# Kernel tuning notes

Hardware: AMD Instinct MI355X
Metric: run time of the kernel (lower is better)

## Reference

```python
import jax, jax.numpy as jnp
import numpy as np

BS, N_LINKS, MAX_LEN = 8192, 512, 32
D_LINK, D_PATH, D_READ, N_OUT = 32, 128, 256, 3
BN_EPS = 1e-5


def setup_inputs() -> dict:
    key = jax.random.key(0)
    ks = jax.random.split(key, 16)
    capa = jax.random.uniform(ks[0], (BS, N_LINKS), jnp.float32, 0.5, 1.0) * 100.0
    avail = jax.random.uniform(ks[1], (BS, N_LINKS), jnp.float32) * capa
    loss = jax.random.uniform(ks[2], (BS, N_LINKS), jnp.float32) * 0.05
    demand = jax.random.uniform(ks[3], (BS,), jnp.float32) * 10.0
    path = jax.random.randint(ks[4], (BS, MAX_LEN), 0, N_LINKS)
    hop_num = jax.random.randint(ks[5], (BS,), 1, MAX_LEN + 1)
    s = 0.1
    inp = {
        "demand": demand,
        "link_avail_capacity": avail,
        "link_capacity": capa,
        "link_loss": loss,
        "path": path,
        "hop_num": hop_num,
        # GRU params (PyTorch layout: [3H, D] gates ordered r,z,n)
        "gru_w_ih": jax.random.normal(ks[6], (3 * D_PATH, D_LINK), jnp.float32) * s,
        "gru_w_hh": jax.random.normal(ks[7], (3 * D_PATH, D_PATH), jnp.float32) * s,
        "gru_b_ih": jax.random.normal(ks[8], (3 * D_PATH,), jnp.float32) * s,
        "gru_b_hh": jax.random.normal(ks[9], (3 * D_PATH,), jnp.float32) * s,
        "bn_gamma": jnp.ones((D_PATH,), jnp.float32),
        "bn_beta": jnp.zeros((D_PATH,), jnp.float32),
        # stacked readout heads [N_OUT, ...]
        "rW1": jax.random.normal(ks[10], (N_OUT, D_PATH, D_READ), jnp.float32) * s,
        "rb1": jnp.zeros((N_OUT, D_READ), jnp.float32),
        "rW2": jax.random.normal(ks[11], (N_OUT, D_READ, D_READ), jnp.float32) * s,
        "rb2": jnp.zeros((N_OUT, D_READ), jnp.float32),
        "rW3": jax.random.normal(ks[12], (N_OUT, D_READ, 1), jnp.float32) * s,
        "rb3": jnp.zeros((N_OUT, 1), jnp.float32),
    }
    return inp


def _gru_scan(x_bt, h0, w_ih, w_hh, b_ih, b_hh):
    # x_bt: [B, T, D]; h0: [B, H] -> outputs [B, T, H]
    H = h0.shape[-1]
    def step(h, x_t):
        gi = x_t @ w_ih.T + b_ih          # [B, 3H]
        gh = h @ w_hh.T + b_hh            # [B, 3H]
        i_r, i_z, i_n = gi[:, :H], gi[:, H:2*H], gi[:, 2*H:]
        h_r, h_z, h_n = gh[:, :H], gh[:, H:2*H], gh[:, 2*H:]
        r = jax.nn.sigmoid(i_r + h_r)
        z = jax.nn.sigmoid(i_z + h_z)
        n = jnp.tanh(i_n + r * h_n)
        h_new = (1.0 - z) * n + z * h
        return h_new, h_new
    _, outs = jax.lax.scan(step, h0, jnp.swapaxes(x_bt, 0, 1))
    return jnp.swapaxes(outs, 0, 1)


def reference(demand, link_avail_capacity, link_capacity, link_loss, path, hop_num,
              gru_w_ih, gru_w_hh, gru_b_ih, gru_b_hh, bn_gamma, bn_beta,
              rW1, rb1, rW2, rb2, rW3, rb3):
    bs, n_links = link_capacity.shape
    max_len = path.shape[1]
    max_capa = jax.lax.stop_gradient(jnp.max(link_capacity))
    # link_state: [B, n_links, D_LINK]; first D_LINK-4 channels are zeros
    feats = jnp.stack([
        link_avail_capacity / max_capa,
        link_capacity / max_capa,
        link_avail_capacity / link_capacity,
        link_loss,
    ], axis=-1)
    link_state = jnp.concatenate(
        [jnp.zeros((bs, n_links, D_LINK - 4), feats.dtype), feats], axis=-1)
    link_state = jax.lax.stop_gradient(link_state)  # original detaches
    # initial hidden: zeros except last channel = demand/max_capa
    h0 = jnp.concatenate(
        [jnp.zeros((bs, D_PATH - 1), feats.dtype), (demand / max_capa)[:, None]], axis=-1)
    # fused gather of link states along each path, masked past hop_num
    gathered = jnp.take_along_axis(link_state, path[:, :, None], axis=1)  # [B, T, D]
    mask = (jnp.arange(max_len)[None, :] < hop_num[:, None])[:, :, None]
    link_inputs = gathered * mask.astype(gathered.dtype)
    outputs = _gru_scan(link_inputs, h0, gru_w_ih, gru_w_hh, gru_b_ih, gru_b_hh)
    # extract hidden state at last hop of each path
    idx = (hop_num - 1)[:, None, None]
    flow = jnp.take_along_axis(outputs, idx, axis=1)[:, 0, :]  # [B, H]
    # BatchNorm1d (training mode: batch statistics, biased variance)
    mean = jnp.mean(flow, axis=0)
    var = jnp.mean((flow - mean) ** 2, axis=0)
    flow = (flow - mean) * jax.lax.rsqrt(var + BN_EPS) * bn_gamma + bn_beta
    # readout heads: Linear -> SELU -> Linear -> SELU -> Linear
    h1 = jax.nn.selu(jnp.einsum('bh,uhr->ubr', flow, rW1) + rb1[:, None, :])
    h2 = jax.nn.selu(jnp.einsum('ubr,urs->ubs', h1, rW2) + rb2[:, None, :])
    y = jnp.einsum('ubs,uso->ubo', h2, rW3) + rb3[:, None, :]  # [U, B, 1]
    return jnp.transpose(y[:, :, 0], (1, 0))  # [B, U]
```

## Files before the change

### kernel.cpp

```cpp
#include <hip/hip_runtime.h>


#define BS 8192
#define NL 512
#define ML 32
#define DP 128
#define DR 256
#define NJOB 512
#define ST 172

#define OFF_SUM    64
#define OFF_SSQ    192
#define OFF_CUR    576
#define OFF_PERM   640
#define OFF_WHH16  (OFF_PERM + BS)
#define OFF_W1     (OFF_WHH16 + 24576)
#define OFF_W2     (OFF_W1 + 49152)
#define OFF_FEATS  (OFF_W2 + 98304)
#define OFF_FLOW   (OFF_FEATS + BS*ML*4)

#define FEATS_BLOCKS 1024
#define MAX_BLOCKS   256
#define WPREP_BLOCKS 336
#define SORT_BID     (FEATS_BLOCKS + MAX_BLOCKS + WPREP_BLOCKS)
#define PREP_GRID    (SORT_BID + 1)

#define KS (-1.44269504088896340736f)
#define KT ( 2.88539008177792681472f)

typedef _Float16 f16x8 __attribute__((ext_vector_type(8)));
typedef _Float16 f16x4 __attribute__((ext_vector_type(4)));
typedef float    f32x4 __attribute__((ext_vector_type(4)));

__device__ __forceinline__ float exp2_raw_(float x){
#if __has_builtin(__builtin_amdgcn_exp2f)
  return __builtin_amdgcn_exp2f(x);
#else
  return exp2f(x);
#endif
}

__device__ __forceinline__ float sig2_(float x){
  return __builtin_amdgcn_rcpf(1.0f + exp2_raw_(x));
}
__device__ __forceinline__ float tanh2_(float v){
  return fmaf(-2.0f, __builtin_amdgcn_rcpf(1.0f + exp2_raw_(v)), 1.0f);
}
__device__ __forceinline__ float seluf_(float x){
  const float sc = 1.0507009873554805f, al = 1.6732632423543772f;
  return x > 0.0f ? sc*x : sc*al*(__expf(x)-1.0f);
}

__global__ void prep_all(const int* __restrict__ path, const int* __restrict__ hop,
                         const float* __restrict__ avail, const float* __restrict__ capa,
                         const float* __restrict__ loss, const float* __restrict__ whh,
                         const float* __restrict__ rW1, const float* __restrict__ rW2,
                         float* ws){
  const int bid = blockIdx.x;
  const int tid = threadIdx.x;

  if (bid < FEATS_BLOCKS){
    int idx = bid*256 + tid;
    int b = idx >> 5, t = idx & 31;
    f16x4 o = (f16x4)0;
    if (t < hop[b]){
      int l = path[idx];
      float a = avail[b*NL + l];
      float c = capa [b*NL + l];
      o[0] = (_Float16)a;
      o[1] = (_Float16)c;
      o[2] = (_Float16)(a / c);
      o[3] = (_Float16)loss[b*NL + l];
    }
    ((f16x4*)((_Float16*)(ws + OFF_FEATS)))[idx] = o;
  } else if (bid < FEATS_BLOCKS + MAX_BLOCKS){
    const float4* c4 = (const float4*)capa;
    const int n4 = BS*NL/4;
    float m = 0.0f;
    for (int i = (bid - FEATS_BLOCKS)*256 + tid; i < n4; i += MAX_BLOCKS*256){
      float4 v = c4[i];
      m = fmaxf(m, fmaxf(fmaxf(v.x, v.y), fmaxf(v.z, v.w)));
    }
    #pragma unroll
    for (int o = 32; o > 0; o >>= 1) m = fmaxf(m, __shfl_down(m, o, 64));
    if ((tid & 63) == 0) atomicMax((int*)ws, __float_as_int(m));
  } else if (bid < SORT_BID){
    _Float16* whh16 = (_Float16*)(ws + OFF_WHH16);
    _Float16* w1    = (_Float16*)(ws + OFF_W1);
    _Float16* w2    = (_Float16*)(ws + OFF_W2);
    int base = (bid - FEATS_BLOCKS - MAX_BLOCKS)*1024 + tid*4;
    if (base < 49152){
      const float s = (base < 32768) ? KS : KT;
      const float4 v = *(const float4*)(whh + base);
      f16x4 o = { (_Float16)(v.x*s), (_Float16)(v.y*s),
                  (_Float16)(v.z*s), (_Float16)(v.w*s) };
      *(f16x4*)(whh16 + base) = o;
    } else if (base < 147456){
      int j = base - 49152; int u = j >> 15; int rem = j & 32767; int n = rem >> 7; int k = rem & 127;
      const float* src = rW1 + u*32768 + k*256 + n;
      f16x4 o = { (_Float16)src[0], (_Float16)src[256], (_Float16)src[512], (_Float16)src[768] };
      *(f16x4*)(w1 + j) = o;
    } else {
      int j = base - 147456; int u = j >> 16; int rem = j & 65535; int n = rem >> 8; int k = rem & 255;
      const float* src = rW2 + u*65536 + k*256 + n;
      f16x4 o = { (_Float16)src[0], (_Float16)src[256], (_Float16)src[512], (_Float16)src[768] };
      *(f16x4*)(w2 + j) = o;
    }
  } else {
    __shared__ int hist[32], start[32];
    for (int i = 64 + tid; i < 640; i += 256) ws[i] = 0.0f;
    if (tid < 32) hist[tid] = 0;
    __syncthreads();
    for (int b = tid; b < BS; b += 256) atomicAdd(&hist[32 - hop[b]], 1);
    __syncthreads();
    if (tid == 0){ int acc = 0; for (int i = 0; i < 32; ++i){ start[i] = acc; acc += hist[i]; } }
    __syncthreads();
    int* perm = (int*)ws + OFF_PERM;
    for (int b = tid; b < BS; b += 256){
      int pos = atomicAdd(&start[32 - hop[b]], 1);
      perm[pos] = b;
    }
  }
}

__launch_bounds__(512, 4)
__global__ void kgru(const float* __restrict__ demand, const int* __restrict__ hop,
                     const float* __restrict__ wih, const float* __restrict__ bih,
                     const float* __restrict__ bhh, float* __restrict__ ws,
                     float* __restrict__ flow){
  __shared__ _Float16 hA[2][16*ST];
  const int tid  = threadIdx.x;
  const int w    = tid >> 6;
  const int lane = tid & 63;
  const int lm   = lane & 15;
  const int qd   = lane >> 4;
  const int ch   = w*16 + lm;
  const float inv_maxc = 1.0f / ws[0];
  const int* perm = (const int*)ws + OFF_PERM;
  const f16x4* feats16 = (const f16x4*)((const _Float16*)(ws + OFF_FEATS));
  const _Float16* whh16 = (const _Float16*)(ws + OFF_WHH16);

  const int bid = blockIdx.x;
  const int q = (bid < 256) ? bid : 767 - bid;

  for (int idx = tid; idx < 1024; idx += 512){
    const int buf = idx >> 9;
    const int rem = idx & 511;
    const int m   = rem >> 5;
    const int c   = 128 + (rem & 31);
    hA[buf][m*ST + c] = (_Float16)0.f;
  }

  f16x8 bfr[5], bfz[5], bfnh[4], bfni;
  #pragma unroll
  for (int kc = 0; kc < 4; ++kc){
    bfr[kc]  = *(const f16x8*)(whh16 + (      ch)*128 + kc*32 + qd*8);
    bfz[kc]  = *(const f16x8*)(whh16 + (128 + ch)*128 + kc*32 + qd*8);
    bfnh[kc] = *(const f16x8*)(whh16 + (256 + ch)*128 + kc*32 + qd*8);
  }
  bfr[4] = (f16x8)0; bfz[4] = (f16x8)0; bfni = (f16x8)0;
  if (qd == 0){
    #pragma unroll
    for (int j = 0; j < 4; ++j){
      float s = (j < 2) ? inv_maxc : 1.0f;
      bfr[4][j] = (_Float16)(wih[(      ch)*32 + 28 + j] * s * KS);
      bfz[4][j] = (_Float16)(wih[(128 + ch)*32 + 28 + j] * s * KS);
      bfni[j]   = (_Float16)(wih[(256 + ch)*32 + 28 + j] * s * KT);
    }
  }
  const float bR  = (bih[ch]     + bhh[ch]    ) * KS;
  const float bZ  = (bih[128+ch] + bhh[128+ch]) * KS;
  const float bNI = bih[256+ch] * KT;
  const float bNH = bhh[256+ch] * KT;

  int it[4], hp[4];
  #pragma unroll
  for (int r = 0; r < 4; ++r){
    it[r] = perm[q*16 + qd*4 + r];
    hp[r] = hop[it[r]];
  }
  int tmax = max(max(hp[0],hp[1]), max(hp[2],hp[3]));
  tmax = max(tmax, __shfl_xor(tmax, 16, 64));
  tmax = max(tmax, __shfl_xor(tmax, 32, 64));

  const int  fw_i = w*2 + lane;
  const bool fw   = (lane < 2);
  const int  fw_b = fw ? perm[q*16 + fw_i] : 0;

  __syncthreads();

  float hprev[4];
  #pragma unroll
  for (int r = 0; r < 4; ++r){
    float h0 = (ch == 127) ? demand[it[r]] * inv_maxc : 0.0f;
    hprev[r] = h0;
    hA[0][(qd*4 + r)*ST + ch] = (_Float16)h0;
  }
  f16x4 fvreg = (f16x4)0;
  if (fw){
    *(f16x4*)(&hA[0][fw_i*ST + 128]) = feats16[fw_b*ML + 0];
    fvreg = feats16[fw_b*ML + 1];
  }
  __syncthreads();

  for (int t = 0; t < tmax; ++t){
    const int cur = t & 1, nxt = cur ^ 1;
    if (fw){
      *(f16x4*)(&hA[nxt][fw_i*ST + 128]) = fvreg;
      int tn = t + 2; tn = (tn < ML) ? tn : (ML - 1);
      fvreg = feats16[fw_b*ML + tn];
    }

    f32x4 accr  = {bR, bR, bR, bR};
    f32x4 accz  = {bZ, bZ, bZ, bZ};
    f32x4 accnh = {bNH, bNH, bNH, bNH};
    f32x4 accni = {bNI, bNI, bNI, bNI};
    #pragma unroll
    for (int kc = 0; kc < 5; ++kc){
      f16x8 a = *(const f16x8*)(&hA[cur][lm*ST + kc*32 + qd*8]);
      accr = __builtin_amdgcn_mfma_f32_16x16x32_f16(a, bfr[kc], accr, 0, 0, 0);
      accz = __builtin_amdgcn_mfma_f32_16x16x32_f16(a, bfz[kc], accz, 0, 0, 0);
      if (kc < 4)
        accnh = __builtin_amdgcn_mfma_f32_16x16x32_f16(a, bfnh[kc], accnh, 0, 0, 0);
      else
        accni = __builtin_amdgcn_mfma_f32_16x16x32_f16(a, bfni, accni, 0, 0, 0);
    }

    #pragma unroll
    for (int r = 0; r < 4; ++r){
      float rr = sig2_(accr[r]);
      float zz = sig2_(accz[r]);
      float nn = tanh2_(fmaf(rr, accnh[r], accni[r]));
      float hn = fmaf(zz, hprev[r] - nn, nn);
      if (t < hp[r]) hprev[r] = hn;
      hA[nxt][(qd*4 + r)*ST + ch] = (_Float16)hprev[r];
    }
    __syncthreads();
  }

  float ssum = 0.f, ssq = 0.f;
  #pragma unroll
  for (int r = 0; r < 4; ++r){
    float v = hprev[r];
    flow[it[r]*DP + ch] = v;
    ssum += v;
    ssq  = fmaf(v, v, ssq);
  }
  ssum += __shfl_xor(ssum, 16, 64);  ssum += __shfl_xor(ssum, 32, 64);
  ssq  += __shfl_xor(ssq,  16, 64);  ssq  += __shfl_xor(ssq,  32, 64);
  if (qd == 0){
    atomicAdd(&ws[OFF_SUM + ch], ssum);
    atomicAdd(&ws[OFF_SSQ + ch], ssq);
  }
}

__launch_bounds__(256, 4)
__global__ void kmlp(const float* __restrict__ flow, const float* __restrict__ ws,
                     const float* __restrict__ gamma, const float* __restrict__ beta,
                     const float* __restrict__ rb1, const float* __restrict__ rb2,
                     const float* __restrict__ rW3, const float* __restrict__ rb3,
                     float* __restrict__ out){
  __shared__ _Float16 x_lds[32*136];
  __shared__ _Float16 h1_lds[32*264];
  __shared__ float aa[DP], bb[DP];
  __shared__ float y_part[4][32];
  const int tid  = threadIdx.x;
  const int w    = tid >> 6;
  const int lane = tid & 63;
  const int lm   = lane & 15;
  const int qd   = lane >> 4;
  const int b0   = blockIdx.x * 32;
  const int u    = blockIdx.y;
  const _Float16* w1 = (const _Float16*)(ws + OFF_W1) + u*(DR*DP);
  const _Float16* w2 = (const _Float16*)(ws + OFF_W2) + u*(DR*DR);

  if (tid < DP){
    float m = ws[OFF_SUM + tid] * (1.0f/BS);
    float q = ws[OFF_SSQ + tid] * (1.0f/BS);
    float rstd = rsqrtf(q - m*m + 1e-5f);
    float a = rstd * gamma[tid];
    aa[tid] = a;
    bb[tid] = fmaf(-m, a, beta[tid]);
  }
  __syncthreads();

  for (int idx = tid; idx < 32*DP; idx += 256){
    int i = idx >> 7, h = idx & 127;
    x_lds[i*136 + h] = (_Float16)fmaf(flow[(b0 + i)*DP + h], aa[h], bb[h]);
  }
  __syncthreads();

  for (int nt = 0; nt < 4; ++nt){
    const int n = (4*w + nt)*16 + lm;
    const float bias1 = rb1[u*DR + n];
    f16x8 b1[4];
    #pragma unroll
    for (int kc = 0; kc < 4; ++kc)
      b1[kc] = *(const f16x8*)(w1 + n*DP + kc*32 + qd*8);
    #pragma unroll
    for (int mt = 0; mt < 2; ++mt){
      f32x4 acc = {bias1, bias1, bias1, bias1};
      #pragma unroll
      for (int kc = 0; kc < 4; ++kc){
        f16x8 a1 = *(const f16x8*)(&x_lds[(mt*16 + lm)*136 + kc*32 + qd*8]);
        acc = __builtin_amdgcn_mfma_f32_16x16x32_f16(a1, b1[kc], acc, 0, 0, 0);
      }
      #pragma unroll
      for (int r = 0; r < 4; ++r)
        h1_lds[(mt*16 + qd*4 + r)*264 + n] = (_Float16)seluf_(acc[r]);
    }
  }
  __syncthreads();

  {
    float p[2][4] = {{0.f,0.f,0.f,0.f},{0.f,0.f,0.f,0.f}};
    for (int nt = 0; nt < 4; ++nt){
      const int n = (4*w + nt)*16 + lm;
      const float bias2 = rb2[u*DR + n];
      const float w3l   = rW3[u*DR + n];
      f16x8 b2[8];
      #pragma unroll
      for (int kc = 0; kc < 8; ++kc)
        b2[kc] = *(const f16x8*)(w2 + n*DR + kc*32 + qd*8);
      #pragma unroll
      for (int mt = 0; mt < 2; ++mt){
        f32x4 acc = {bias2, bias2, bias2, bias2};
        #pragma unroll
        for (int kc = 0; kc < 8; ++kc){
          f16x8 a2 = *(const f16x8*)(&h1_lds[(mt*16 + lm)*264 + kc*32 + qd*8]);
          acc = __builtin_amdgcn_mfma_f32_16x16x32_f16(a2, b2[kc], acc, 0, 0, 0);
        }
        #pragma unroll
        for (int r = 0; r < 4; ++r)
          p[mt][r] += seluf_(acc[r]) * w3l;
      }
    }
    #pragma unroll
    for (int mt = 0; mt < 2; ++mt){
      #pragma unroll
      for (int r = 0; r < 4; ++r){
        float v = p[mt][r];
        v += __shfl_xor(v, 1, 64);
        v += __shfl_xor(v, 2, 64);
        v += __shfl_xor(v, 4, 64);
        v += __shfl_xor(v, 8, 64);
        if (lm == 0) y_part[w][mt*16 + qd*4 + r] = v;
      }
    }
  }
  __syncthreads();
  if (tid < 32){
    float y = y_part[0][tid] + y_part[1][tid] + y_part[2][tid] + y_part[3][tid] + rb3[u];
    out[(b0 + tid)*3 + u] = y;
  }
}

extern "C" void kernel_launch(void* const* d_in, const int* in_sizes, int n_in,
                              void* d_out, int out_size, void* d_ws, size_t ws_size,
                              hipStream_t stream){
  const float* demand = (const float*)d_in[0];
  const float* avail  = (const float*)d_in[1];
  const float* capa   = (const float*)d_in[2];
  const float* loss   = (const float*)d_in[3];
  const int*   path   = (const int*)d_in[4];
  const int*   hop    = (const int*)d_in[5];
  const float* wih    = (const float*)d_in[6];
  const float* whh    = (const float*)d_in[7];
  const float* bih    = (const float*)d_in[8];
  const float* bhh    = (const float*)d_in[9];
  const float* gamma  = (const float*)d_in[10];
  const float* beta   = (const float*)d_in[11];
  const float* rW1    = (const float*)d_in[12];
  const float* rb1    = (const float*)d_in[13];
  const float* rW2    = (const float*)d_in[14];
  const float* rb2    = (const float*)d_in[15];
  const float* rW3    = (const float*)d_in[16];
  const float* rb3    = (const float*)d_in[17];
  float* ws  = (float*)d_ws;
  float* out = (float*)d_out;

  prep_all <<<PREP_GRID, 256, 0, stream>>>(path, hop, avail, capa, loss,
                                           whh, rW1, rW2, ws);
  kgru     <<<NJOB, 512, 0, stream>>>(demand, hop, wih, bih, bhh, ws, ws + OFF_FLOW);
  kmlp     <<<dim3(BS/32, 3), 256, 0, stream>>>(ws + OFF_FLOW, ws, gamma, beta,
                                                rb1, rb2, rW3, rb3, out);
}
```

Before: 196.9 us.

## Halve GRU block to 4 waves, each computing two 16-channel slices

The GRU kernel now launches 256 threads per block instead of 512. Each wave covers 32 hidden channels as two 16-channel slices and reuses one set of A-fragment LDS loads for both slices' MFMAs. This is meant to cut LDS reads and barrier cost per timestep and to give each wave more independent MFMA work to hide latency. In exchange, per-wave register pressure roughly doubles for the weight fragments, the launch bound drops to 2 blocks per CU, and the serial chain per wave grows.

```diff
diff --git a/kernel.cpp b/kernel.cpp
--- a/kernel.cpp
+++ b/kernel.cpp
@@ -123,7 +123,7 @@
   }
 }
 
-__launch_bounds__(512, 4)
+__launch_bounds__(256, 2)
 __global__ void kgru(const float* __restrict__ demand, const int* __restrict__ hop,
                      const float* __restrict__ wih, const float* __restrict__ bih,
                      const float* __restrict__ bhh, float* __restrict__ ws,
@@ -134,7 +134,8 @@
   const int lane = tid & 63;
   const int lm   = lane & 15;
   const int qd   = lane >> 4;
-  const int ch   = w*16 + lm;
+  const int ch0  = w*32 + lm;
+  const int ch1  = w*32 + 16 + lm;
   const float inv_maxc = 1.0f / ws[0];
   const int* perm = (const int*)ws + OFF_PERM;
   const f16x4* feats16 = (const f16x4*)((const _Float16*)(ws + OFF_FEATS));
@@ -143,7 +144,7 @@
   const int bid = blockIdx.x;
   const int q = (bid < 256) ? bid : 767 - bid;
 
-  for (int idx = tid; idx < 1024; idx += 512){
+  for (int idx = tid; idx < 1024; idx += 256){
     const int buf = idx >> 9;
     const int rem = idx & 511;
     const int m   = rem >> 5;
@@ -151,27 +152,35 @@
     hA[buf][m*ST + c] = (_Float16)0.f;
   }
 
-  f16x8 bfr[5], bfz[5], bfnh[4], bfni;
+  f16x8 bfr[2][5], bfz[2][5], bfnh[2][4], bfni[2];
   #pragma unroll
-  for (int kc = 0; kc < 4; ++kc){
-    bfr[kc]  = *(const f16x8*)(whh16 + (      ch)*128 + kc*32 + qd*8);
-    bfz[kc]  = *(const f16x8*)(whh16 + (128 + ch)*128 + kc*32 + qd*8);
-    bfnh[kc] = *(const f16x8*)(whh16 + (256 + ch)*128 + kc*32 + qd*8);
-  }
-  bfr[4] = (f16x8)0; bfz[4] = (f16x8)0; bfni = (f16x8)0;
-  if (qd == 0){
-    #pragma unroll
-    for (int j = 0; j < 4; ++j){
-      float s = (j < 2) ? inv_maxc : 1.0f;
-      bfr[4][j] = (_Float16)(wih[(      ch)*32 + 28 + j] * s * KS);
-      bfz[4][j] = (_Float16)(wih[(128 + ch)*32 + 28 + j] * s * KS);
-      bfni[j]   = (_Float16)(wih[(256 + ch)*32 + 28 + j] * s * KT);
-    }
-  }
-  const float bR  = (bih[ch]     + bhh[ch]    ) * KS;
-  const float bZ  = (bih[128+ch] + bhh[128+ch]) * KS;
-  const float bNI = bih[256+ch] * KT;
-  const float bNH = bhh[256+ch] * KT;
+  for (int s = 0; s < 2; ++s){
+    const int chs = w*32 + s*16 + lm;
+    #pragma unroll
+    for (int kc = 0; kc < 4; ++kc){
+      bfr[s][kc]  = *(const f16x8*)(whh16 + (      chs)*128 + kc*32 + qd*8);
+      bfz[s][kc]  = *(const f16x8*)(whh16 + (128 + chs)*128 + kc*32 + qd*8);
+      bfnh[s][kc] = *(const f16x8*)(whh16 + (256 + chs)*128 + kc*32 + qd*8);
+    }
+    bfr[s][4] = (f16x8)0; bfz[s][4] = (f16x8)0; bfni[s] = (f16x8)0;
+    if (qd == 0){
+      #pragma unroll
+      for (int j = 0; j < 4; ++j){
+        float sc = (j < 2) ? inv_maxc : 1.0f;
+        bfr[s][4][j] = (_Float16)(wih[(      chs)*32 + 28 + j] * sc * KS);
+        bfz[s][4][j] = (_Float16)(wih[(128 + chs)*32 + 28 + j] * sc * KS);
+        bfni[s][j]   = (_Float16)(wih[(256 + chs)*32 + 28 + j] * sc * KT);
+      }
+    }
+  }
+  const float bR0  = (bih[ch0]     + bhh[ch0]    ) * KS;
+  const float bR1  = (bih[ch1]     + bhh[ch1]    ) * KS;
+  const float bZ0  = (bih[128+ch0] + bhh[128+ch0]) * KS;
+  const float bZ1  = (bih[128+ch1] + bhh[128+ch1]) * KS;
+  const float bNI0 = bih[256+ch0] * KT;
+  const float bNI1 = bih[256+ch1] * KT;
+  const float bNH0 = bhh[256+ch0] * KT;
+  const float bNH1 = bhh[256+ch1] * KT;
 
   int it[4], hp[4];
   #pragma unroll
@@ -183,18 +192,19 @@
   tmax = max(tmax, __shfl_xor(tmax, 16, 64));
   tmax = max(tmax, __shfl_xor(tmax, 32, 64));
 
-  const int  fw_i = w*2 + lane;
-  const bool fw   = (lane < 2);
+  const int  fw_i = w*4 + lane;
+  const bool fw   = (lane < 4);
   const int  fw_b = fw ? perm[q*16 + fw_i] : 0;
 
   __syncthreads();
 
-  float hprev[4];
+  float hprev0[4], hprev1[4];
   #pragma unroll
   for (int r = 0; r < 4; ++r){
-    float h0 = (ch == 127) ? demand[it[r]] * inv_maxc : 0.0f;
-    hprev[r] = h0;
-    hA[0][(qd*4 + r)*ST + ch] = (_Float16)h0;
+    hprev0[r] = 0.0f;
+    hprev1[r] = (ch1 == 127) ? demand[it[r]] * inv_maxc : 0.0f;
+    hA[0][(qd*4 + r)*ST + ch0] = (_Float16)hprev0[r];
+    hA[0][(qd*4 + r)*ST + ch1] = (_Float16)hprev1[r];
   }
   f16x4 fvreg = (f16x4)0;
   if (fw){
@@ -211,46 +221,80 @@
       fvreg = feats16[fw_b*ML + tn];
     }
 
-    f32x4 accr  = {bR, bR, bR, bR};
-    f32x4 accz  = {bZ, bZ, bZ, bZ};
-    f32x4 accnh = {bNH, bNH, bNH, bNH};
-    f32x4 accni = {bNI, bNI, bNI, bNI};
-    #pragma unroll
-    for (int kc = 0; kc < 5; ++kc){
-      f16x8 a = *(const f16x8*)(&hA[cur][lm*ST + kc*32 + qd*8]);
-      accr = __builtin_amdgcn_mfma_f32_16x16x32_f16(a, bfr[kc], accr, 0, 0, 0);
-      accz = __builtin_amdgcn_mfma_f32_16x16x32_f16(a, bfz[kc], accz, 0, 0, 0);
-      if (kc < 4)
-        accnh = __builtin_amdgcn_mfma_f32_16x16x32_f16(a, bfnh[kc], accnh, 0, 0, 0);
-      else
-        accni = __builtin_amdgcn_mfma_f32_16x16x32_f16(a, bfni, accni, 0, 0, 0);
-    }
-
-    #pragma unroll
-    for (int r = 0; r < 4; ++r){
-      float rr = sig2_(accr[r]);
-      float zz = sig2_(accz[r]);
-      float nn = tanh2_(fmaf(rr, accnh[r], accni[r]));
-      float hn = fmaf(zz, hprev[r] - nn, nn);
-      if (t < hp[r]) hprev[r] = hn;
-      hA[nxt][(qd*4 + r)*ST + ch] = (_Float16)hprev[r];
+    f16x8 a[5];
+    #pragma unroll
+    for (int kc = 0; kc < 5; ++kc)
+      a[kc] = *(const f16x8*)(&hA[cur][lm*ST + kc*32 + qd*8]);
+
+    {
+      f32x4 accr  = {bR0, bR0, bR0, bR0};
+      f32x4 accz  = {bZ0, bZ0, bZ0, bZ0};
+      f32x4 accnh = {bNH0, bNH0, bNH0, bNH0};
+      f32x4 accni = {bNI0, bNI0, bNI0, bNI0};
+      #pragma unroll
+      for (int kc = 0; kc < 5; ++kc){
+        accr = __builtin_amdgcn_mfma_f32_16x16x32_f16(a[kc], bfr[0][kc], accr, 0, 0, 0);
+        accz = __builtin_amdgcn_mfma_f32_16x16x32_f16(a[kc], bfz[0][kc], accz, 0, 0, 0);
+        if (kc < 4)
+          accnh = __builtin_amdgcn_mfma_f32_16x16x32_f16(a[kc], bfnh[0][kc], accnh, 0, 0, 0);
+        else
+          accni = __builtin_amdgcn_mfma_f32_16x16x32_f16(a[kc], bfni[0], accni, 0, 0, 0);
+      }
+      #pragma unroll
+      for (int r = 0; r < 4; ++r){
+        float rr = sig2_(accr[r]);
+        float zz = sig2_(accz[r]);
+        float nn = tanh2_(fmaf(rr, accnh[r], accni[r]));
+        float hn = fmaf(zz, hprev0[r] - nn, nn);
+        if (t < hp[r]) hprev0[r] = hn;
+        hA[nxt][(qd*4 + r)*ST + ch0] = (_Float16)hprev0[r];
+      }
+    }
+    {
+      f32x4 accr  = {bR1, bR1, bR1, bR1};
+      f32x4 accz  = {bZ1, bZ1, bZ1, bZ1};
+      f32x4 accnh = {bNH1, bNH1, bNH1, bNH1};
+      f32x4 accni = {bNI1, bNI1, bNI1, bNI1};
+      #pragma unroll
+      for (int kc = 0; kc < 5; ++kc){
+        accr = __builtin_amdgcn_mfma_f32_16x16x32_f16(a[kc], bfr[1][kc], accr, 0, 0, 0);
+        accz = __builtin_amdgcn_mfma_f32_16x16x32_f16(a[kc], bfz[1][kc], accz, 0, 0, 0);
+        if (kc < 4)
+          accnh = __builtin_amdgcn_mfma_f32_16x16x32_f16(a[kc], bfnh[1][kc], accnh, 0, 0, 0);
+        else
+          accni = __builtin_amdgcn_mfma_f32_16x16x32_f16(a[kc], bfni[1], accni, 0, 0, 0);
+      }
+      #pragma unroll
+      for (int r = 0; r < 4; ++r){
+        float rr = sig2_(accr[r]);
+        float zz = sig2_(accz[r]);
+        float nn = tanh2_(fmaf(rr, accnh[r], accni[r]));
+        float hn = fmaf(zz, hprev1[r] - nn, nn);
+        if (t < hp[r]) hprev1[r] = hn;
+        hA[nxt][(qd*4 + r)*ST + ch1] = (_Float16)hprev1[r];
+      }
     }
     __syncthreads();
   }
 
-  float ssum = 0.f, ssq = 0.f;
+  float s0 = 0.f, q0 = 0.f, s1 = 0.f, q1 = 0.f;
   #pragma unroll
   for (int r = 0; r < 4; ++r){
-    float v = hprev[r];
-    flow[it[r]*DP + ch] = v;
-    ssum += v;
-    ssq  = fmaf(v, v, ssq);
-  }
-  ssum += __shfl_xor(ssum, 16, 64);  ssum += __shfl_xor(ssum, 32, 64);
-  ssq  += __shfl_xor(ssq,  16, 64);  ssq  += __shfl_xor(ssq,  32, 64);
+    float v0 = hprev0[r], v1 = hprev1[r];
+    flow[it[r]*DP + ch0] = v0;
+    flow[it[r]*DP + ch1] = v1;
+    s0 += v0;  q0 = fmaf(v0, v0, q0);
+    s1 += v1;  q1 = fmaf(v1, v1, q1);
+  }
+  s0 += __shfl_xor(s0, 16, 64);  s0 += __shfl_xor(s0, 32, 64);
+  q0 += __shfl_xor(q0, 16, 64);  q0 += __shfl_xor(q0, 32, 64);
+  s1 += __shfl_xor(s1, 16, 64);  s1 += __shfl_xor(s1, 32, 64);
+  q1 += __shfl_xor(q1, 16, 64);  q1 += __shfl_xor(q1, 32, 64);
   if (qd == 0){
-    atomicAdd(&ws[OFF_SUM + ch], ssum);
-    atomicAdd(&ws[OFF_SSQ + ch], ssq);
+    atomicAdd(&ws[OFF_SUM + ch0], s0);
+    atomicAdd(&ws[OFF_SSQ + ch0], q0);
+    atomicAdd(&ws[OFF_SUM + ch1], s1);
+    atomicAdd(&ws[OFF_SSQ + ch1], q1);
   }
 }
 
@@ -381,7 +425,7 @@
 
   prep_all <<<PREP_GRID, 256, 0, stream>>>(path, hop, avail, capa, loss,
                                            whh, rW1, rW2, ws);
-  kgru     <<<NJOB, 512, 0, stream>>>(demand, hop, wih, bih, bhh, ws, ws + OFF_FLOW);
+  kgru     <<<NJOB, 256, 0, stream>>>(demand, hop, wih, bih, bhh, ws, ws + OFF_FLOW);
   kmlp     <<<dim3(BS/32, 3), 256, 0, stream>>>(ws + OFF_FLOW, ws, gamma, beta,
                                                 rb1, rb2, rW3, rb3, out);
 }
```

New measurement: 197.0 us. About the same (+0.0%).
